# Kernel tuning notes

Hardware: AMD Instinct MI355X
Metric: run time of the kernel (lower is better)

## Reference

```python
import jax, jax.numpy as jnp
import numpy as np


def _segment_softmax(x, seg, num_segments):
    # x: (E, C), seg: (E,) int. Numerically stable per-segment softmax along dim 0.
    m = jax.ops.segment_max(x, seg, num_segments=num_segments)  # (S, C)
    # Guard empty segments (-inf) so gather stays finite for used rows.
    e = jnp.exp(x - m[seg])                                     # (E, C)
    s = jax.ops.segment_sum(e, seg, num_segments=num_segments)  # (S, C)
    return e / s[seg]


def setup_inputs() -> dict:
    key = jax.random.key(0)
    k1, k2, k3, k4 = jax.random.split(key, 4)
    E, C, S = 16777216, 2, 4096
    return {
        "xab": jax.random.normal(k1, (E, C), dtype=jnp.float32),
        "xba": jax.random.normal(k2, (E, C), dtype=jnp.float32),
        "src_id": jax.random.randint(k3, (E,), 0, S, dtype=jnp.int64),
        "tar_id": jax.random.randint(k4, (E,), 0, S, dtype=jnp.int64),
        "num_segments": S,
    }


def reference(xab, xba, src_id, tar_id, num_segments):
    zab = _segment_softmax(xab, src_id, num_segments)  # softmax over src groups
    zba = _segment_softmax(xba, tar_id, num_segments)  # softmax over tar groups
    return (zab * zba, zab, zba)
```

## Files before the change

kernel.cpp:

```cpp
#include <hip/hip_runtime.h>

#define NSEG 4096
#define QSCALE 131072.0f
#define QINV   (1.0f / 131072.0f)

typedef unsigned long long u64;
typedef unsigned int u32;
typedef float f32x4 __attribute__((ext_vector_type(4)));
typedef float f32x2 __attribute__((ext_vector_type(2)));

__global__ __launch_bounds__(1024) void dsp_reduce(
    const f32x4* __restrict__ xab4, const f32x4* __restrict__ xba4,
    const int2* __restrict__ src2, const int2* __restrict__ tar2,
    float* __restrict__ partials,
    float* __restrict__ gtab,
    int Eh)
{
    __shared__ u64 ls[2 * NSEG];
    for (int i = threadIdx.x; i < 2 * NSEG; i += 1024) ls[i] = 0ull;
    __syncthreads();

    const int stride = gridDim.x * 1024;
    int u = blockIdx.x * 1024 + threadIdx.x;

    f32x4 a, b; int2 s, t;
    if (u < Eh) { a = xab4[u]; b = xba4[u]; s = src2[u]; t = tar2[u]; }

    while (u < Eh) {
        int un = u + stride;
        f32x4 an, bn; int2 sn, tn;
        if (un < Eh) { an = xab4[un]; bn = xba4[un]; sn = src2[un]; tn = tar2[un]; }

        u32 a0 = __float2uint_rn(__expf(a.x) * QSCALE);
        u32 a1 = __float2uint_rn(__expf(a.y) * QSCALE);
        u32 a2 = __float2uint_rn(__expf(a.z) * QSCALE);
        u32 a3 = __float2uint_rn(__expf(a.w) * QSCALE);
        atomicAdd(&ls[s.x], (u64)a0 | ((u64)a1 << 32));
        atomicAdd(&ls[s.y], (u64)a2 | ((u64)a3 << 32));

        u32 b0 = __float2uint_rn(__expf(b.x) * QSCALE);
        u32 b1 = __float2uint_rn(__expf(b.y) * QSCALE);
        u32 b2 = __float2uint_rn(__expf(b.z) * QSCALE);
        u32 b3 = __float2uint_rn(__expf(b.w) * QSCALE);
        atomicAdd(&ls[NSEG + t.x], (u64)b0 | ((u64)b1 << 32));
        atomicAdd(&ls[NSEG + t.y], (u64)b2 | ((u64)b3 << 32));

        u = un; a = an; b = bn; s = sn; t = tn;
    }
    __syncthreads();

    if (partials) {
        f32x2* dst = (f32x2*)(partials + (size_t)blockIdx.x * (4 * NSEG));
        for (int i = threadIdx.x; i < 2 * NSEG; i += 1024) {
            u64 v = ls[i];
            f32x2 w = { (float)(u32)v * QINV, (float)(u32)(v >> 32) * QINV };
            dst[i] = w;
        }
    } else {
        for (int i = threadIdx.x; i < 2 * NSEG; i += 1024) {
            u64 v = ls[i];
            float lo = (float)(u32)v * QINV;
            float hi = (float)(u32)(v >> 32) * QINV;
            if (lo != 0.f) atomicAdd(&gtab[2 * i], lo);
            if (hi != 0.f) atomicAdd(&gtab[2 * i + 1], hi);
        }
    }
}

__global__ __launch_bounds__(256) void dsp_sum(
    const f32x4* __restrict__ partials, f32x4* __restrict__ rcp_out, int nb)
{
    int i = blockIdx.x * blockDim.x + threadIdx.x;
    f32x4 acc = {0.f, 0.f, 0.f, 0.f};
    for (int p = 0; p < nb; ++p) {
        f32x4 v = __builtin_nontemporal_load(&partials[(size_t)p * NSEG + i]);
        acc += v;
    }
    f32x4 r;
    r.x = (acc.x > 0.f) ? 1.f / acc.x : 0.f;
    r.y = (acc.y > 0.f) ? 1.f / acc.y : 0.f;
    r.z = (acc.z > 0.f) ? 1.f / acc.z : 0.f;
    r.w = (acc.w > 0.f) ? 1.f / acc.w : 0.f;
    rcp_out[i] = r;
}

__global__ void dsp_rcp(float* __restrict__ sums, int n)
{
    int i = blockIdx.x * blockDim.x + threadIdx.x;
    if (i < n) {
        float v = sums[i];
        sums[i] = (v > 0.f) ? 1.f / v : 0.f;
    }
}

__global__ __launch_bounds__(1024) void dsp_norm(
    const f32x4* __restrict__ xab4, const f32x4* __restrict__ xba4,
    const int2* __restrict__ src2, const int2* __restrict__ tar2,
    const f32x4* __restrict__ rcp_tab,
    f32x4* __restrict__ out, int Eh)
{
    __shared__ float ls[4 * NSEG];
    for (int i = threadIdx.x; i < NSEG; i += 1024)
        ((f32x4*)ls)[i] = rcp_tab[i];
    __syncthreads();

    const int stride = gridDim.x * 1024;
    int u = blockIdx.x * 1024 + threadIdx.x;

    f32x4 a, b; int2 s, t;
    if (u < Eh) { a = xab4[u]; b = xba4[u]; s = src2[u]; t = tar2[u]; }

    while (u < Eh) {
        int un = u + stride;
        f32x4 an, bn; int2 sn, tn;
        if (un < Eh) { an = xab4[un]; bn = xba4[un]; sn = src2[un]; tn = tar2[un]; }

        f32x2 ra0 = *(const f32x2*)&ls[2 * s.x];
        f32x2 ra1 = *(const f32x2*)&ls[2 * s.y];
        f32x2 rb0 = *(const f32x2*)&ls[2 * NSEG + 2 * t.x];
        f32x2 rb1 = *(const f32x2*)&ls[2 * NSEG + 2 * t.y];

        f32x4 zab = { __expf(a.x) * ra0.x, __expf(a.y) * ra0.y,
                      __expf(a.z) * ra1.x, __expf(a.w) * ra1.y };
        f32x4 zba = { __expf(b.x) * rb0.x, __expf(b.y) * rb0.y,
                      __expf(b.z) * rb1.x, __expf(b.w) * rb1.y };
        f32x4 prod = zab * zba;

        __builtin_nontemporal_store(prod, &out[u]);
        __builtin_nontemporal_store(zab,  &out[Eh + u]);
        __builtin_nontemporal_store(zba,  &out[2 * Eh + u]);

        u = un; a = an; b = bn; s = sn; t = tn;
    }
}

extern "C" void kernel_launch(void* const* d_in, const int* in_sizes, int n_in,
                              void* d_out, int out_size, void* d_ws, size_t ws_size,
                              hipStream_t stream)
{
    const int E  = in_sizes[0] / 2;
    const int Eh = E / 2;
    const f32x4* xab4 = (const f32x4*)d_in[0];
    const f32x4* xba4 = (const f32x4*)d_in[1];
    const int2*  src2 = (const int2*)d_in[2];
    const int2*  tar2 = (const int2*)d_in[3];

    const int NB = 512;
    float* rcp_tab  = (float*)d_ws;
    float* partials = (float*)((char*)d_ws + 65536);
    size_t need = 65536 + (size_t)NB * 65536;

    if (ws_size >= need) {
        dsp_reduce<<<NB, 1024, 0, stream>>>(xab4, xba4, src2, tar2,
                                            partials, nullptr, Eh);
        dsp_sum<<<NSEG / 256, 256, 0, stream>>>((const f32x4*)partials,
                                                (f32x4*)rcp_tab, NB);
    } else {
        (void)hipMemsetAsync(d_ws, 0, 65536, stream);
        dsp_reduce<<<NB, 1024, 0, stream>>>(xab4, xba4, src2, tar2,
                                            nullptr, rcp_tab, Eh);
        dsp_rcp<<<64, 256, 0, stream>>>(rcp_tab, 4 * NSEG);
    }

    dsp_norm<<<512, 1024, 0, stream>>>(xab4, xba4, src2, tar2,
                                       (const f32x4*)rcp_tab,
                                       (f32x4*)d_out, Eh);
}
```

Baseline: 356.8 us.

## Traverse reduce pass in reverse so normalize pass reuses cached inputs

The reduction kernel now walks its grid-stride rounds from last to first, using an exact round count that has no bounds checks. The normalize kernel walks them first to last. The inputs read most recently by the reduction are therefore read first by normalization, which is meant to hit in the last-level (infinity) cache instead of going back to HBM. Partial writes also become nontemporal stores. The non-exact fallback now always writes per-block partials, even when the workspace may be too small for them, which is a correctness risk on that path.

```diff
diff --git a/kernel.cpp b/kernel.cpp
--- a/kernel.cpp
+++ b/kernel.cpp
@@ -9,27 +9,26 @@
 typedef float f32x4 __attribute__((ext_vector_type(4)));
 typedef float f32x2 __attribute__((ext_vector_type(2)));
 
-__global__ __launch_bounds__(1024) void dsp_reduce(
+__global__ __launch_bounds__(1024) void dsp_reduce_x(
     const f32x4* __restrict__ xab4, const f32x4* __restrict__ xba4,
     const int2* __restrict__ src2, const int2* __restrict__ tar2,
     float* __restrict__ partials,
-    float* __restrict__ gtab,
-    int Eh)
+    int rounds, int rs)
 {
     __shared__ u64 ls[2 * NSEG];
     for (int i = threadIdx.x; i < 2 * NSEG; i += 1024) ls[i] = 0ull;
     __syncthreads();
 
-    const int stride = gridDim.x * 1024;
-    int u = blockIdx.x * 1024 + threadIdx.x;
-
-    f32x4 a, b; int2 s, t;
-    if (u < Eh) { a = xab4[u]; b = xba4[u]; s = src2[u]; t = tar2[u]; }
-
-    while (u < Eh) {
-        int un = u + stride;
+    const int base = blockIdx.x * 1024 + threadIdx.x;
+    int u = base + (rounds - 1) * rs;
+
+    f32x4 a = xab4[u], b = xba4[u];
+    int2 s = src2[u], t = tar2[u];
+
+    for (int r = rounds - 1; r >= 0; --r) {
+        int un = u - rs;
         f32x4 an, bn; int2 sn, tn;
-        if (un < Eh) { an = xab4[un]; bn = xba4[un]; sn = src2[un]; tn = tar2[un]; }
+        if (r > 0) { an = xab4[un]; bn = xba4[un]; sn = src2[un]; tn = tar2[un]; }
 
         u32 a0 = __float2uint_rn(__expf(a.x) * QSCALE);
         u32 a1 = __float2uint_rn(__expf(a.y) * QSCALE);
@@ -49,21 +48,47 @@
     }
     __syncthreads();
 
-    if (partials) {
-        f32x2* dst = (f32x2*)(partials + (size_t)blockIdx.x * (4 * NSEG));
-        for (int i = threadIdx.x; i < 2 * NSEG; i += 1024) {
-            u64 v = ls[i];
-            f32x2 w = { (float)(u32)v * QINV, (float)(u32)(v >> 32) * QINV };
-            dst[i] = w;
-        }
-    } else {
-        for (int i = threadIdx.x; i < 2 * NSEG; i += 1024) {
-            u64 v = ls[i];
-            float lo = (float)(u32)v * QINV;
-            float hi = (float)(u32)(v >> 32) * QINV;
-            if (lo != 0.f) atomicAdd(&gtab[2 * i], lo);
-            if (hi != 0.f) atomicAdd(&gtab[2 * i + 1], hi);
-        }
+    f32x2* dst = (f32x2*)(partials + (size_t)blockIdx.x * (4 * NSEG));
+    for (int i = threadIdx.x; i < 2 * NSEG; i += 1024) {
+        u64 v = ls[i];
+        f32x2 w = { (float)(u32)v * QINV, (float)(u32)(v >> 32) * QINV };
+        __builtin_nontemporal_store(w, &dst[i]);
+    }
+}
+
+__global__ __launch_bounds__(1024) void dsp_reduce_g(
+    const f32x4* __restrict__ xab4, const f32x4* __restrict__ xba4,
+    const int2* __restrict__ src2, const int2* __restrict__ tar2,
+    float* __restrict__ partials, int Eh)
+{
+    __shared__ u64 ls[2 * NSEG];
+    for (int i = threadIdx.x; i < 2 * NSEG; i += 1024) ls[i] = 0ull;
+    __syncthreads();
+
+    const int stride = gridDim.x * 1024;
+    for (int u = blockIdx.x * 1024 + threadIdx.x; u < Eh; u += stride) {
+        f32x4 a = xab4[u]; f32x4 b = xba4[u];
+        int2 s = src2[u]; int2 t = tar2[u];
+        u32 a0 = __float2uint_rn(__expf(a.x) * QSCALE);
+        u32 a1 = __float2uint_rn(__expf(a.y) * QSCALE);
+        u32 a2 = __float2uint_rn(__expf(a.z) * QSCALE);
+        u32 a3 = __float2uint_rn(__expf(a.w) * QSCALE);
+        atomicAdd(&ls[s.x], (u64)a0 | ((u64)a1 << 32));
+        atomicAdd(&ls[s.y], (u64)a2 | ((u64)a3 << 32));
+        u32 b0 = __float2uint_rn(__expf(b.x) * QSCALE);
+        u32 b1 = __float2uint_rn(__expf(b.y) * QSCALE);
+        u32 b2 = __float2uint_rn(__expf(b.z) * QSCALE);
+        u32 b3 = __float2uint_rn(__expf(b.w) * QSCALE);
+        atomicAdd(&ls[NSEG + t.x], (u64)b0 | ((u64)b1 << 32));
+        atomicAdd(&ls[NSEG + t.y], (u64)b2 | ((u64)b3 << 32));
+    }
+    __syncthreads();
+
+    f32x2* dst = (f32x2*)(partials + (size_t)blockIdx.x * (4 * NSEG));
+    for (int i = threadIdx.x; i < 2 * NSEG; i += 1024) {
+        u64 v = ls[i];
+        f32x2 w = { (float)(u32)v * QINV, (float)(u32)(v >> 32) * QINV };
+        __builtin_nontemporal_store(w, &dst[i]);
     }
 }
 
@@ -84,36 +109,27 @@
     rcp_out[i] = r;
 }
 
-__global__ void dsp_rcp(float* __restrict__ sums, int n)
-{
-    int i = blockIdx.x * blockDim.x + threadIdx.x;
-    if (i < n) {
-        float v = sums[i];
-        sums[i] = (v > 0.f) ? 1.f / v : 0.f;
-    }
-}
-
-__global__ __launch_bounds__(1024) void dsp_norm(
+__global__ __launch_bounds__(1024) void dsp_norm_x(
     const f32x4* __restrict__ xab4, const f32x4* __restrict__ xba4,
     const int2* __restrict__ src2, const int2* __restrict__ tar2,
     const f32x4* __restrict__ rcp_tab,
-    f32x4* __restrict__ out, int Eh)
+    f32x4* __restrict__ out, int rounds, int rs, int Eh)
 {
     __shared__ float ls[4 * NSEG];
     for (int i = threadIdx.x; i < NSEG; i += 1024)
         ((f32x4*)ls)[i] = rcp_tab[i];
     __syncthreads();
 
-    const int stride = gridDim.x * 1024;
-    int u = blockIdx.x * 1024 + threadIdx.x;
-
-    f32x4 a, b; int2 s, t;
-    if (u < Eh) { a = xab4[u]; b = xba4[u]; s = src2[u]; t = tar2[u]; }
-
-    while (u < Eh) {
-        int un = u + stride;
+    const int base = blockIdx.x * 1024 + threadIdx.x;
+    int u = base;
+
+    f32x4 a = xab4[u], b = xba4[u];
+    int2 s = src2[u], t = tar2[u];
+
+    for (int r = 0; r < rounds; ++r) {
+        int un = u + rs;
         f32x4 an, bn; int2 sn, tn;
-        if (un < Eh) { an = xab4[un]; bn = xba4[un]; sn = src2[un]; tn = tar2[un]; }
+        if (r + 1 < rounds) { an = xab4[un]; bn = xba4[un]; sn = src2[un]; tn = tar2[un]; }
 
         f32x2 ra0 = *(const f32x2*)&ls[2 * s.x];
         f32x2 ra1 = *(const f32x2*)&ls[2 * s.y];
@@ -131,6 +147,36 @@
         __builtin_nontemporal_store(zba,  &out[2 * Eh + u]);
 
         u = un; a = an; b = bn; s = sn; t = tn;
+    }
+}
+
+__global__ __launch_bounds__(1024) void dsp_norm_g(
+    const f32x4* __restrict__ xab4, const f32x4* __restrict__ xba4,
+    const int2* __restrict__ src2, const int2* __restrict__ tar2,
+    const f32x4* __restrict__ rcp_tab,
+    f32x4* __restrict__ out, int Eh)
+{
+    __shared__ float ls[4 * NSEG];
+    for (int i = threadIdx.x; i < NSEG; i += 1024)
+        ((f32x4*)ls)[i] = rcp_tab[i];
+    __syncthreads();
+
+    const int stride = gridDim.x * 1024;
+    for (int u = blockIdx.x * 1024 + threadIdx.x; u < Eh; u += stride) {
+        f32x4 a = xab4[u]; f32x4 b = xba4[u];
+        int2 s = src2[u]; int2 t = tar2[u];
+        f32x2 ra0 = *(const f32x2*)&ls[2 * s.x];
+        f32x2 ra1 = *(const f32x2*)&ls[2 * s.y];
+        f32x2 rb0 = *(const f32x2*)&ls[2 * NSEG + 2 * t.x];
+        f32x2 rb1 = *(const f32x2*)&ls[2 * NSEG + 2 * t.y];
+        f32x4 zab = { __expf(a.x) * ra0.x, __expf(a.y) * ra0.y,
+                      __expf(a.z) * ra1.x, __expf(a.w) * ra1.y };
+        f32x4 zba = { __expf(b.x) * rb0.x, __expf(b.y) * rb0.y,
+                      __expf(b.z) * rb1.x, __expf(b.w) * rb1.y };
+        f32x4 prod = zab * zba;
+        __builtin_nontemporal_store(prod, &out[u]);
+        __builtin_nontemporal_store(zab,  &out[Eh + u]);
+        __builtin_nontemporal_store(zba,  &out[2 * Eh + u]);
     }
 }
 
@@ -146,23 +192,28 @@
     const int2*  tar2 = (const int2*)d_in[3];
 
     const int NB = 512;
+    const int RS = NB * 1024;
     float* rcp_tab  = (float*)d_ws;
     float* partials = (float*)((char*)d_ws + 65536);
     size_t need = 65536 + (size_t)NB * 65536;
-
-    if (ws_size >= need) {
-        dsp_reduce<<<NB, 1024, 0, stream>>>(xab4, xba4, src2, tar2,
-                                            partials, nullptr, Eh);
+    const bool exact = (ws_size >= need) && (Eh % RS == 0) && (Eh / RS >= 1);
+
+    if (exact) {
+        const int rounds = Eh / RS;
+        dsp_reduce_x<<<NB, 1024, 0, stream>>>(xab4, xba4, src2, tar2,
+                                              partials, rounds, RS);
         dsp_sum<<<NSEG / 256, 256, 0, stream>>>((const f32x4*)partials,
                                                 (f32x4*)rcp_tab, NB);
+        dsp_norm_x<<<NB, 1024, 0, stream>>>(xab4, xba4, src2, tar2,
+                                            (const f32x4*)rcp_tab,
+                                            (f32x4*)d_out, rounds, RS, Eh);
     } else {
-        (void)hipMemsetAsync(d_ws, 0, 65536, stream);
-        dsp_reduce<<<NB, 1024, 0, stream>>>(xab4, xba4, src2, tar2,
-                                            nullptr, rcp_tab, Eh);
-        dsp_rcp<<<64, 256, 0, stream>>>(rcp_tab, 4 * NSEG);
-    }
-
-    dsp_norm<<<512, 1024, 0, stream>>>(xab4, xba4, src2, tar2,
-                                       (const f32x4*)rcp_tab,
-                                       (f32x4*)d_out, Eh);
-}
+        dsp_reduce_g<<<NB, 1024, 0, stream>>>(xab4, xba4, src2, tar2,
+                                              partials, Eh);
+        dsp_sum<<<NSEG / 256, 256, 0, stream>>>((const f32x4*)partials,
+                                                (f32x4*)rcp_tab, NB);
+        dsp_norm_g<<<NB, 1024, 0, stream>>>(xab4, xba4, src2, tar2,
+                                            (const f32x4*)rcp_tab,
+                                            (f32x4*)d_out, Eh);
+    }
+}
```

Result: slower. 429.1 us (+20.3%).

## Route tar-side segment sums to global u64 atomics, halve per-block partials

Applied to the files above, without the earlier changes.

The tar-group exponential sums are now accumulated with 64-bit atomics directly in a small global table, and only the src-group sums stay in shared-memory per-block partials. This halves the per-block partial buffer that is written and later re-read by the summing kernel, and halves LDS use per block. It also drops the manual software prefetch in the reduce loop. The trade-off is heavy contention from global atomics on 4096 addresses over millions of edges, which may serialize in L2, and an extra memset and kernel launch.

```diff
diff --git a/kernel.cpp b/kernel.cpp
--- a/kernel.cpp
+++ b/kernel.cpp
@@ -3,6 +3,7 @@
 #define NSEG 4096
 #define QSCALE 131072.0f
 #define QINV   (1.0f / 131072.0f)
+#define NB 512
 
 typedef unsigned long long u64;
 typedef unsigned int u32;
@@ -13,84 +14,77 @@
     const f32x4* __restrict__ xab4, const f32x4* __restrict__ xba4,
     const int2* __restrict__ src2, const int2* __restrict__ tar2,
     float* __restrict__ partials,
-    float* __restrict__ gtab,
+    u64* __restrict__ gab,
+    u64* __restrict__ gba,
     int Eh)
 {
-    __shared__ u64 ls[2 * NSEG];
-    for (int i = threadIdx.x; i < 2 * NSEG; i += 1024) ls[i] = 0ull;
+    __shared__ u64 ls[NSEG];
+    for (int i = threadIdx.x; i < NSEG; i += 1024) ls[i] = 0ull;
     __syncthreads();
 
     const int stride = gridDim.x * 1024;
-    int u = blockIdx.x * 1024 + threadIdx.x;
+    for (int u = blockIdx.x * 1024 + threadIdx.x; u < Eh; u += stride) {
+        f32x4 a = xab4[u];
+        f32x4 b = xba4[u];
+        int2 s = src2[u];
+        int2 t = tar2[u];
 
-    f32x4 a, b; int2 s, t;
-    if (u < Eh) { a = xab4[u]; b = xba4[u]; s = src2[u]; t = tar2[u]; }
-
-    while (u < Eh) {
-        int un = u + stride;
-        f32x4 an, bn; int2 sn, tn;
-        if (un < Eh) { an = xab4[un]; bn = xba4[un]; sn = src2[un]; tn = tar2[un]; }
+        u32 b0 = __float2uint_rn(__expf(b.x) * QSCALE);
+        u32 b1 = __float2uint_rn(__expf(b.y) * QSCALE);
+        u32 b2 = __float2uint_rn(__expf(b.z) * QSCALE);
+        u32 b3 = __float2uint_rn(__expf(b.w) * QSCALE);
+        atomicAdd(&gba[t.x], (u64)b0 | ((u64)b1 << 32));
+        atomicAdd(&gba[t.y], (u64)b2 | ((u64)b3 << 32));
 
         u32 a0 = __float2uint_rn(__expf(a.x) * QSCALE);
         u32 a1 = __float2uint_rn(__expf(a.y) * QSCALE);
         u32 a2 = __float2uint_rn(__expf(a.z) * QSCALE);
         u32 a3 = __float2uint_rn(__expf(a.w) * QSCALE);
-        atomicAdd(&ls[s.x], (u64)a0 | ((u64)a1 << 32));
-        atomicAdd(&ls[s.y], (u64)a2 | ((u64)a3 << 32));
-
-        u32 b0 = __float2uint_rn(__expf(b.x) * QSCALE);
-        u32 b1 = __float2uint_rn(__expf(b.y) * QSCALE);
-        u32 b2 = __float2uint_rn(__expf(b.z) * QSCALE);
-        u32 b3 = __float2uint_rn(__expf(b.w) * QSCALE);
-        atomicAdd(&ls[NSEG + t.x], (u64)b0 | ((u64)b1 << 32));
-        atomicAdd(&ls[NSEG + t.y], (u64)b2 | ((u64)b3 << 32));
-
-        u = un; a = an; b = bn; s = sn; t = tn;
+        if (partials) {
+            atomicAdd(&ls[s.x], (u64)a0 | ((u64)a1 << 32));
+            atomicAdd(&ls[s.y], (u64)a2 | ((u64)a3 << 32));
+        } else {
+            atomicAdd(&gab[s.x], (u64)a0 | ((u64)a1 << 32));
+            atomicAdd(&gab[s.y], (u64)a2 | ((u64)a3 << 32));
+        }
     }
     __syncthreads();
 
     if (partials) {
-        f32x2* dst = (f32x2*)(partials + (size_t)blockIdx.x * (4 * NSEG));
-        for (int i = threadIdx.x; i < 2 * NSEG; i += 1024) {
+        f32x2* dst = (f32x2*)(partials + (size_t)blockIdx.x * (2 * NSEG));
+        for (int i = threadIdx.x; i < NSEG; i += 1024) {
             u64 v = ls[i];
             f32x2 w = { (float)(u32)v * QINV, (float)(u32)(v >> 32) * QINV };
             dst[i] = w;
         }
-    } else {
-        for (int i = threadIdx.x; i < 2 * NSEG; i += 1024) {
-            u64 v = ls[i];
-            float lo = (float)(u32)v * QINV;
-            float hi = (float)(u32)(v >> 32) * QINV;
-            if (lo != 0.f) atomicAdd(&gtab[2 * i], lo);
-            if (hi != 0.f) atomicAdd(&gtab[2 * i + 1], hi);
-        }
     }
 }
 
-__global__ __launch_bounds__(256) void dsp_sum(
-    const f32x4* __restrict__ partials, f32x4* __restrict__ rcp_out, int nb)
+__global__ __launch_bounds__(256) void dsp_sum_ab(
+    const f32x4* __restrict__ partials, f32x4* __restrict__ rcp_ab, int nb)
 {
     int i = blockIdx.x * blockDim.x + threadIdx.x;
     f32x4 acc = {0.f, 0.f, 0.f, 0.f};
-    for (int p = 0; p < nb; ++p) {
-        f32x4 v = __builtin_nontemporal_load(&partials[(size_t)p * NSEG + i]);
-        acc += v;
-    }
+    for (int p = 0; p < nb; ++p)
+        acc += partials[(size_t)p * (NSEG / 2) + i];
     f32x4 r;
     r.x = (acc.x > 0.f) ? 1.f / acc.x : 0.f;
     r.y = (acc.y > 0.f) ? 1.f / acc.y : 0.f;
     r.z = (acc.z > 0.f) ? 1.f / acc.z : 0.f;
     r.w = (acc.w > 0.f) ? 1.f / acc.w : 0.f;
-    rcp_out[i] = r;
+    rcp_ab[i] = r;
 }
 
-__global__ void dsp_rcp(float* __restrict__ sums, int n)
+__global__ __launch_bounds__(256) void dsp_sum_u64(
+    const u64* __restrict__ gtab, f32x2* __restrict__ rcp_out)
 {
-    int i = blockIdx.x * blockDim.x + threadIdx.x;
-    if (i < n) {
-        float v = sums[i];
-        sums[i] = (v > 0.f) ? 1.f / v : 0.f;
-    }
+    int j = blockIdx.x * blockDim.x + threadIdx.x;
+    u64 v = gtab[j];
+    float lo = (float)(u32)v * QINV;
+    float hi = (float)(u32)(v >> 32) * QINV;
+    f32x2 r = { (lo > 0.f) ? 1.f / lo : 0.f,
+                (hi > 0.f) ? 1.f / hi : 0.f };
+    rcp_out[j] = r;
 }
 
 __global__ __launch_bounds__(1024) void dsp_norm(
@@ -145,24 +139,31 @@
     const int2*  src2 = (const int2*)d_in[2];
     const int2*  tar2 = (const int2*)d_in[3];
 
-    const int NB = 512;
     float* rcp_tab  = (float*)d_ws;
-    float* partials = (float*)((char*)d_ws + 65536);
-    size_t need = 65536 + (size_t)NB * 65536;
+    u64*   gba      = (u64*)((char*)d_ws + 65536);
+    u64*   gab      = (u64*)((char*)d_ws + 65536 + 32768);
+    float* partials = (float*)((char*)d_ws + 65536 + 2 * 32768);
+    size_t need = 65536 + 2 * 32768 + (size_t)NB * (2 * NSEG) * sizeof(float);
 
     if (ws_size >= need) {
+        (void)hipMemsetAsync(gba, 0, 32768, stream);
         dsp_reduce<<<NB, 1024, 0, stream>>>(xab4, xba4, src2, tar2,
-                                            partials, nullptr, Eh);
-        dsp_sum<<<NSEG / 256, 256, 0, stream>>>((const f32x4*)partials,
-                                                (f32x4*)rcp_tab, NB);
+                                            partials, nullptr, gba, Eh);
+        dsp_sum_ab<<<(NSEG / 2) / 256, 256, 0, stream>>>(
+            (const f32x4*)partials, (f32x4*)rcp_tab, NB);
+        dsp_sum_u64<<<NSEG / 256, 256, 0, stream>>>(
+            gba, (f32x2*)(rcp_tab + 2 * NSEG));
     } else {
-        (void)hipMemsetAsync(d_ws, 0, 65536, stream);
+        (void)hipMemsetAsync(gba, 0, 2 * 32768, stream);
         dsp_reduce<<<NB, 1024, 0, stream>>>(xab4, xba4, src2, tar2,
-                                            nullptr, rcp_tab, Eh);
-        dsp_rcp<<<64, 256, 0, stream>>>(rcp_tab, 4 * NSEG);
+                                            nullptr, gab, gba, Eh);
+        dsp_sum_u64<<<NSEG / 256, 256, 0, stream>>>(
+            gab, (f32x2*)rcp_tab);
+        dsp_sum_u64<<<NSEG / 256, 256, 0, stream>>>(
+            gba, (f32x2*)(rcp_tab + 2 * NSEG));
     }
 
-    dsp_norm<<<512, 1024, 0, stream>>>(xab4, xba4, src2, tar2,
-                                       (const f32x4*)rcp_tab,
-                                       (f32x4*)d_out, Eh);
+    dsp_norm<<<NB, 1024, 0, stream>>>(xab4, xba4, src2, tar2,
+                                      (const f32x4*)rcp_tab,
+                                      (f32x4*)d_out, Eh);
 }
```

After: 972.3 us. 2.72x slower.
